# Performance work log

Measured on AMD Instinct MI355X. Metric: run time of the kernel, lower is better.

Reference implementation:

```python
import jax, jax.numpy as jnp
import numpy as np

B, D = 8192, 256      # batch, input_dim == n_nodes
ENC = 256             # encoder_dim
DEC = 64              # decoder_dim
THR = 0.1             # adjacency threshold


def setup_inputs() -> dict:
    key = jax.random.key(0)
    ks = jax.random.split(key, 9)
    s = lambda k, sh, fan: jax.random.normal(k, sh, jnp.float32) / np.sqrt(fan).astype(np.float32)
    return {
        "x": jax.random.normal(ks[0], (B, D), jnp.float32),
        "eps": jax.random.normal(ks[1], (B, D), jnp.float32),
        "W_enc": s(ks[2], (D, ENC), D), "b_enc": jnp.zeros((ENC,), jnp.float32),
        "W_mu": s(ks[3], (ENC, D), ENC), "b_mu": jnp.zeros((D,), jnp.float32),
        "W_lv": s(ks[4], (ENC, D), ENC), "b_lv": jnp.zeros((D,), jnp.float32),
        "graph_param": jax.random.normal(ks[5], (D, D), jnp.float32),
        "W_emb": s(ks[6], (D, DEC), 1), "b_emb": jnp.zeros((D, DEC), jnp.float32),
        "W_g1": s(ks[7], (DEC, DEC // 2), DEC), "b_g1": jnp.zeros((DEC // 2,), jnp.float32),
        "W_g2": s(ks[8], (DEC // 2, 1), DEC // 2), "b_g2": jnp.zeros((1,), jnp.float32),
        "iter_": 100,
    }


def _learned_graph(graph_param, iter_):
    # LearnedGraph.forward: sigmoid, force self-loops=1, threshold after iter 50
    g = jax.nn.sigmoid(graph_param)
    eye = jnp.eye(g.shape[0], dtype=g.dtype)
    g = g * (1.0 - eye) + eye
    if iter_ > 50:  # iter_ is a static Python int
        g = jnp.where(g > THR, g, 0.0)  # nn.Threshold(THR, 0)
    return g


def _gcn_norm(adj):
    # DGL GraphConv(norm='both') with edge_weight: messages weighted by adj values,
    # but degree normalization uses structural (unweighted) edge counts.
    mask = (adj != 0).astype(adj.dtype)
    dout = jnp.maximum(mask.sum(1), 1.0)  # out-degree of src j (row sums)
    din = jnp.maximum(mask.sum(0), 1.0)   # in-degree of dst i (col sums)
    # out[i] = sum_j adj[j,i] * x[j] / sqrt(dout[j] * din[i])  ->  M[dst, src]
    return (adj / jnp.sqrt(dout)[:, None] / jnp.sqrt(din)[None, :]).T


def reference(x, eps, W_enc, b_enc, W_mu, b_mu, W_lv, b_lv,
              graph_param, W_emb, b_emb, W_g1, b_g1, W_g2, b_g2, iter_):
    # VAE encoder (Linear + ReLU, then mu/logvar heads)
    h = jax.nn.relu(x @ W_enc + b_enc)
    mu = h @ W_mu + b_mu
    logvar = h @ W_lv + b_lv
    z = mu + eps * jnp.exp(0.5 * logvar)                 # [B, D]
    # learned adjacency over the D feature-nodes
    adj = _learned_graph(graph_param, iter_)             # [D, D]
    # per-feature node embedding: Linear(1, DEC) + tanh per feature
    b_z = jnp.tanh(z[:, :, None] * W_emb[None] + b_emb[None])  # [B, D, DEC]
    # two GraphConv layers (shared adjacency per batch element)
    M = _gcn_norm(adj)                                   # [D, D]
    h1 = jax.nn.relu(jnp.einsum('ij,bjd->bid', M, b_z) @ W_g1 + b_g1)  # [B, D, 32]
    h2 = jnp.einsum('ij,bjd->bid', M, h1) @ W_g2 + b_g2                # [B, D, 1]
    x_hat = h2.reshape(B, -1)                            # [B, D]
    return x_hat, adj, mu, logvar
```

## Files before the change

kernel.cpp:

```cpp
#include <hip/hip_runtime.h>

typedef __bf16 bf16_t;
typedef __bf16 bf16x4 __attribute__((ext_vector_type(4)));
typedef __bf16 bf16x8 __attribute__((ext_vector_type(8)));
typedef float  floatx4 __attribute__((ext_vector_type(4)));

#define MFMA16(a, b, c) __builtin_amdgcn_mfma_f32_16x16x32_bf16((a), (b), (c), 0, 0, 0)

#define ADJ_OFF  2097152
#define MU_OFF   2162688
#define LV_OFF   4259840

#define TWO_LOG2E 2.8853900817779268f

__device__ __forceinline__ float fast_tanh2(float argE2) {
    float e = __builtin_amdgcn_exp2f(argE2);
    return 1.0f - 2.0f * __builtin_amdgcn_rcpf(e + 1.0f);
}

__device__ __forceinline__ bf16x8 cvt8(const float* p) {
    const floatx4 a = *(const floatx4*)p;
    const floatx4 b = *(const floatx4*)(p + 4);
    bf16x8 r;
#pragma unroll
    for (int j = 0; j < 4; j++) { r[j] = (bf16_t)a[j]; r[4 + j] = (bf16_t)b[j]; }
    return r;
}

__global__ __launch_bounds__(256) void k_prep(
    const float* __restrict__ We, const float* __restrict__ Wm,
    const float* __restrict__ Wl, const float* __restrict__ Wemb,
    const float* __restrict__ bemb, bf16_t* __restrict__ Wt,
    bf16_t* __restrict__ wepack, bf16_t* __restrict__ bepack,
    int* __restrict__ colc) {
    __shared__ float tile[32][33];
    const int b = blockIdx.x, tid = threadIdx.x;
    if (b < 192) {
        const int m = b >> 6, t6 = b & 63;
        const int K0 = (t6 >> 3) << 5, N0 = (t6 & 7) << 5;
        const float* src = (m == 0) ? We : ((m == 1) ? Wm : Wl);
#pragma unroll
        for (int p = 0; p < 4; p++) {
            const int idx = p * 256 + tid;
            tile[idx >> 5][idx & 31] = src[(K0 + (idx >> 5)) * 256 + N0 + (idx & 31)];
        }
        __syncthreads();
        bf16_t* dst = Wt + m * 65536;
#pragma unroll
        for (int p = 0; p < 4; p++) {
            const int idx = p * 256 + tid;
            const int nn = idx >> 5, kk = idx & 31;
            dst[(N0 + nn) * 256 + K0 + kk] = (bf16_t)tile[kk][nn];
        }
    } else if (b < 200) {
        const int base = (b - 192) * 2048;
#pragma unroll
        for (int p = 0; p < 8; p++) {
            const int idx = base + p * 256 + tid;
            wepack[idx] = (bf16_t)(TWO_LOG2E * Wemb[idx]);
        }
    } else {
        if (b == 200) colc[tid] = 0;
        const int base = (b - 200) * 2048;
#pragma unroll
        for (int p = 0; p < 8; p++) {
            const int idx = base + p * 256 + tid;
            bepack[idx] = (bf16_t)(TWO_LOG2E * bemb[idx]);
        }
    }
}

__global__ __launch_bounds__(256) void k_deg(
    const float* __restrict__ gp, const int* __restrict__ iterp,
    int* __restrict__ colc, float* __restrict__ rsO) {
    __shared__ unsigned long long mk[4];
    const int j = blockIdx.x, t = threadIdx.x;
    const bool thr = (*iterp) > 50;
    float g = 1.0f / (1.0f + expf(-gp[j * 256 + t]));
    if (t == j) g = 1.0f;
    if (thr && !(g > 0.1f)) g = 0.0f;
    const bool nz = (g != 0.0f);
    const unsigned long long bal = __ballot(nz);
    if ((t & 63) == 0) mk[t >> 6] = bal;
    if (nz) atomicAdd(&colc[t], 1);
    __syncthreads();
    if (t == 0) {
        const int rc = (int)(__popcll(mk[0]) + __popcll(mk[1]) +
                             __popcll(mk[2]) + __popcll(mk[3]));
        rsO[j] = rsqrtf((float)(rc < 1 ? 1 : rc));
    }
}

__global__ __launch_bounds__(256) void k_mkM(
    const float* __restrict__ gp, const int* __restrict__ iterp,
    const int* __restrict__ colc, const float* __restrict__ rsO,
    bf16_t* __restrict__ Mb, float* __restrict__ adjOut) {
    const int j = blockIdx.x, t = threadIdx.x;
    const int ci = colc[t];
    const float rsi = rsqrtf((float)(ci < 1 ? 1 : ci));
    float g = 1.0f / (1.0f + expf(-gp[j * 256 + t]));
    if (t == j) g = 1.0f;
    if ((*iterp) > 50 && !(g > 0.1f)) g = 0.0f;
    if (adjOut) adjOut[j * 256 + t] = g;
    Mb[t * 256 + j] = (bf16_t)(g * rsO[j] * rsi);
}

__global__ __launch_bounds__(512) void k_ench(
    const float* __restrict__ X, const bf16_t* __restrict__ Wt,
    const float* __restrict__ benc, const float* __restrict__ bmu,
    const float* __restrict__ blv,
    float* __restrict__ MuOut, float* __restrict__ LvOut) {
    __shared__ __align__(16) bf16_t Xs[32 * 264];
    __shared__ __align__(16) bf16_t Hs[32 * 264];
    const bf16_t* Bte = Wt;
    const bf16_t* Btm = Wt + 65536;
    const bf16_t* Btl = Wt + 131072;
    const int tid = threadIdx.x;
    const int r0 = blockIdx.x * 32;
    const int w = tid >> 6;
    const int lane = tid & 63;
    const int n = lane & 15, q = lane >> 4;
    const int cw = w * 32;
    const floatx4 z4 = {0.f, 0.f, 0.f, 0.f};

#pragma unroll
    for (int p = 0; p < 2; p++) {
        const int e0 = (p * 512 + tid) * 8;
        const int row = e0 >> 8, col = e0 & 255;
        *(bf16x8*)(Xs + row * 264 + col) = cvt8(X + (r0 + row) * 256 + col);
    }
    __syncthreads();

    floatx4 ah[2][2];
#pragma unroll
    for (int rt = 0; rt < 2; rt++)
#pragma unroll
        for (int tc = 0; tc < 2; tc++) ah[rt][tc] = z4;
#pragma unroll 2
    for (int k0 = 0; k0 < 256; k0 += 32) {
        bf16x8 a[2], b[2];
#pragma unroll
        for (int rt = 0; rt < 2; rt++)
            a[rt] = *(const bf16x8*)(Xs + (rt * 16 + n) * 264 + k0 + q * 8);
#pragma unroll
        for (int tc = 0; tc < 2; tc++)
            b[tc] = *(const bf16x8*)(Bte + (cw + tc * 16 + n) * 256 + k0 + q * 8);
#pragma unroll
        for (int rt = 0; rt < 2; rt++)
#pragma unroll
            for (int tc = 0; tc < 2; tc++)
                ah[rt][tc] = MFMA16(a[rt], b[tc], ah[rt][tc]);
    }
#pragma unroll
    for (int tc = 0; tc < 2; tc++) {
        const int col = cw + tc * 16 + n;
        const float bv = benc[col];
#pragma unroll
        for (int rt = 0; rt < 2; rt++)
#pragma unroll
            for (int r = 0; r < 4; r++)
                Hs[(rt * 16 + q * 4 + r) * 264 + col] =
                    (bf16_t)fmaxf(ah[rt][tc][r] + bv, 0.0f);
    }
    __syncthreads();

    floatx4 am[2][2], al[2][2];
#pragma unroll
    for (int rt = 0; rt < 2; rt++)
#pragma unroll
        for (int tc = 0; tc < 2; tc++) { am[rt][tc] = z4; al[rt][tc] = z4; }
#pragma unroll 2
    for (int k0 = 0; k0 < 256; k0 += 32) {
        bf16x8 a[2], bm_[2], bl_[2];
#pragma unroll
        for (int rt = 0; rt < 2; rt++)
            a[rt] = *(const bf16x8*)(Hs + (rt * 16 + n) * 264 + k0 + q * 8);
#pragma unroll
        for (int tc = 0; tc < 2; tc++) {
            bm_[tc] = *(const bf16x8*)(Btm + (cw + tc * 16 + n) * 256 + k0 + q * 8);
            bl_[tc] = *(const bf16x8*)(Btl + (cw + tc * 16 + n) * 256 + k0 + q * 8);
        }
#pragma unroll
        for (int rt = 0; rt < 2; rt++)
#pragma unroll
            for (int tc = 0; tc < 2; tc++) {
                am[rt][tc] = MFMA16(a[rt], bm_[tc], am[rt][tc]);
                al[rt][tc] = MFMA16(a[rt], bl_[tc], al[rt][tc]);
            }
    }
#pragma unroll
    for (int tc = 0; tc < 2; tc++) {
        const int col = cw + tc * 16 + n;
        const float bmv = bmu[col], blvv = blv[col];
#pragma unroll
        for (int rt = 0; rt < 2; rt++)
#pragma unroll
            for (int r = 0; r < 4; r++) {
                const int row = r0 + rt * 16 + q * 4 + r;
                MuOut[row * 256 + col] = am[rt][tc][r] + bmv;
                LvOut[row * 256 + col] = al[rt][tc][r] + blvv;
            }
    }
}

__global__ __launch_bounds__(512, 4) void k_gcn(
    const float* __restrict__ Mu, const float* __restrict__ Lv,
    const float* __restrict__ Eps, const bf16_t* __restrict__ wepack,
    const bf16_t* __restrict__ bepack, const float* __restrict__ Wg1,
    const float* __restrict__ bg1, const float* __restrict__ Wg2,
    const bf16_t* __restrict__ Mb, float* __restrict__ Vout) {
    __shared__ __align__(16) bf16_t smem[128 * 256];
    __shared__ float zs[1024];
    const int tid = threadIdx.x;
    const int lane = tid & 63;
    const int w = tid >> 6;
    const int n = lane & 15, q = lane >> 4;
    const int bg = blockIdx.x;
    const floatx4 z4 = {0.f, 0.f, 0.f, 0.f};

    {
        const int gi = bg * 1024 + tid;
        zs[tid] = fmaf(Eps[gi], __expf(0.5f * Lv[gi]), Mu[gi]);
        const int gi2 = gi + 512;
        zs[tid + 512] = fmaf(Eps[gi2], __expf(0.5f * Lv[gi2]), Mu[gi2]);
    }

    bf16x8 wg1f[2][2];
#pragma unroll
    for (int ks = 0; ks < 2; ks++)
#pragma unroll
        for (int te = 0; te < 2; te++)
#pragma unroll
            for (int j = 0; j < 8; j++)
                wg1f[ks][te][j] = (bf16_t)Wg1[(ks * 32 + q * 8 + j) * 32 + te * 16 + n];
    __syncthreads();

#pragma unroll
    for (int jt2 = 0; jt2 < 2; jt2++) {
        const int j0 = (w * 2 + jt2) * 16;
        const int jA = j0 + n;
        const bf16x8 we0 = *(const bf16x8*)(wepack + jA * 64 + q * 8);
        const bf16x8 we1 = *(const bf16x8*)(wepack + jA * 64 + 32 + q * 8);
        const bf16x8 be0 = *(const bf16x8*)(bepack + jA * 64 + q * 8);
        const bf16x8 be1 = *(const bf16x8*)(bepack + jA * 64 + 32 + q * 8);
        float wf0[8], wf1[8], bf0[8], bf1[8];
#pragma unroll
        for (int j = 0; j < 8; j++) {
            wf0[j] = (float)we0[j]; wf1[j] = (float)we1[j];
            bf0[j] = (float)be0[j]; bf1[j] = (float)be1[j];
        }
        const int j8a = (j0 >> 3) + (q >> 1);
        const int jlo = (q & 1) * 4;
        const int sw = ((j8a ^ (n & 7)) << 3) + jlo;
#pragma unroll
        for (int bl = 0; bl < 4; bl++) {
            const float zv = zs[bl * 256 + jA];
            bf16x8 a0, a1;
#pragma unroll
            for (int j = 0; j < 8; j++) {
                a0[j] = (bf16_t)fast_tanh2(fmaf(zv, wf0[j], bf0[j]));
                a1[j] = (bf16_t)fast_tanh2(fmaf(zv, wf1[j], bf1[j]));
            }
            floatx4 c0 = z4, c1 = z4;
            c0 = MFMA16(a0, wg1f[0][0], c0);
            c0 = MFMA16(a1, wg1f[1][0], c0);
            c1 = MFMA16(a0, wg1f[0][1], c1);
            c1 = MFMA16(a1, wg1f[1][1], c1);
            bf16x4 s0, s1;
#pragma unroll
            for (int r = 0; r < 4; r++) { s0[r] = (bf16_t)c0[r]; s1[r] = (bf16_t)c1[r]; }
            *(bf16x4*)(smem + (bl * 32 + n) * 256 + sw) = s0;
            *(bf16x4*)(smem + (bl * 32 + 16 + n) * 256 + sw) = s1;
        }
    }
    __syncthreads();

    const int i0 = w * 32;
    floatx4 acc[2][8];
#pragma unroll
    for (int ti = 0; ti < 2; ti++)
#pragma unroll
        for (int tc = 0; tc < 8; tc++) acc[ti][tc] = z4;
#pragma unroll
    for (int k0 = 0; k0 < 256; k0 += 32) {
        const int k8 = k0 >> 3;
        bf16x8 a[2], b[8];
#pragma unroll
        for (int ti = 0; ti < 2; ti++)
            a[ti] = *(const bf16x8*)(Mb + (i0 + ti * 16 + n) * 256 + k0 + q * 8);
#pragma unroll
        for (int tc = 0; tc < 8; tc++)
            b[tc] = *(const bf16x8*)(smem + (tc * 16 + n) * 256 +
                                     (((k8 + q) ^ (n & 7)) << 3));
        __builtin_amdgcn_s_setprio(1);
#pragma unroll
        for (int ti = 0; ti < 2; ti++)
#pragma unroll
            for (int tc = 0; tc < 8; tc++)
                acc[ti][tc] = MFMA16(a[ti], b[tc], acc[ti][tc]);
        __builtin_amdgcn_s_setprio(0);
    }

    const float w2a = Wg2[n],      w2b = Wg2[16 + n];
    const float b1a = bg1[n],      b1b = bg1[16 + n];
    float v32[32];
#pragma unroll
    for (int bl = 0; bl < 4; bl++)
#pragma unroll
        for (int ti = 0; ti < 2; ti++)
#pragma unroll
            for (int r = 0; r < 4; r++)
                v32[bl * 8 + ti * 4 + r] =
                    fmaxf(acc[ti][2 * bl][r] + b1a, 0.0f) * w2a +
                    fmaxf(acc[ti][2 * bl + 1][r] + b1b, 0.0f) * w2b;
    const bool h0 = (lane & 1), h1_ = (lane & 2), h2 = (lane & 4), h3 = (lane & 8);
    float u16[16];
#pragma unroll
    for (int p = 0; p < 16; p++) {
        const float keep = h0 ? v32[2 * p + 1] : v32[2 * p];
        const float send = h0 ? v32[2 * p] : v32[2 * p + 1];
        u16[p] = keep + __shfl_xor(send, 1, 64);
    }
    float u8[8];
#pragma unroll
    for (int p = 0; p < 8; p++) {
        const float keep = h1_ ? u16[2 * p + 1] : u16[2 * p];
        const float send = h1_ ? u16[2 * p] : u16[2 * p + 1];
        u8[p] = keep + __shfl_xor(send, 2, 64);
    }
    float u4[4];
#pragma unroll
    for (int p = 0; p < 4; p++) {
        const float keep = h2 ? u8[2 * p + 1] : u8[2 * p];
        const float send = h2 ? u8[2 * p] : u8[2 * p + 1];
        u4[p] = keep + __shfl_xor(send, 4, 64);
    }
    float u2[2];
#pragma unroll
    for (int p = 0; p < 2; p++) {
        const float keep = h3 ? u4[2 * p + 1] : u4[2 * p];
        const float send = h3 ? u4[2 * p] : u4[2 * p + 1];
        u2[p] = keep + __shfl_xor(send, 8, 64);
    }
    {
        const int i_out = i0 + ((n >> 2) & 1) * 16 + q * 4 + (n & 3);
        const int blv = n >> 3;
        Vout[bg * 1024 + blv * 256 + i_out] = u2[0];
        Vout[bg * 1024 + (2 + blv) * 256 + i_out] = u2[1];
    }
}

__global__ __launch_bounds__(512) void k_out(
    float* __restrict__ VX, const bf16_t* __restrict__ Mb,
    const float* __restrict__ bg2) {
    __shared__ __align__(16) bf16_t va[32 * 264];
    const int tid = threadIdx.x;
    const int lane = tid & 63;
    const int w = tid >> 6;
    const int n = lane & 15, q = lane >> 4;
    const int r0 = blockIdx.x * 32;

#pragma unroll
    for (int p = 0; p < 4; p++) {
        const int i4 = p * 512 + tid;
        const int row = i4 >> 6, c4 = (i4 & 63) * 4;
        const floatx4 v = *(const floatx4*)(VX + (r0 + row) * 256 + c4);
        bf16x4 s;
#pragma unroll
        for (int r = 0; r < 4; r++) s[r] = (bf16_t)v[r];
        *(bf16x4*)(va + row * 264 + c4) = s;
    }
    __syncthreads();

    const int cw = w * 32;
    const floatx4 z4 = {0.f, 0.f, 0.f, 0.f};
    floatx4 acc[2][2];
#pragma unroll
    for (int rt = 0; rt < 2; rt++)
#pragma unroll
        for (int tc = 0; tc < 2; tc++) acc[rt][tc] = z4;
#pragma unroll 2
    for (int k0 = 0; k0 < 256; k0 += 32) {
        bf16x8 a[2], b[2];
#pragma unroll
        for (int rt = 0; rt < 2; rt++)
            a[rt] = *(const bf16x8*)(va + (rt * 16 + n) * 264 + k0 + q * 8);
#pragma unroll
        for (int tc = 0; tc < 2; tc++)
            b[tc] = *(const bf16x8*)(Mb + (cw + tc * 16 + n) * 256 + k0 + q * 8);
#pragma unroll
        for (int rt = 0; rt < 2; rt++)
#pragma unroll
            for (int tc = 0; tc < 2; tc++)
                acc[rt][tc] = MFMA16(a[rt], b[tc], acc[rt][tc]);
    }
    const float bv = bg2[0];
#pragma unroll
    for (int tc = 0; tc < 2; tc++) {
        const int col = cw + tc * 16 + n;
#pragma unroll
        for (int rt = 0; rt < 2; rt++)
#pragma unroll
            for (int r = 0; r < 4; r++)
                VX[(r0 + rt * 16 + q * 4 + r) * 256 + col] = acc[rt][tc][r] + bv;
    }
}

__global__ __launch_bounds__(256) void k_adj(
    const float* __restrict__ gp, const int* __restrict__ iterp,
    float* __restrict__ adjOut) {
    const int o = blockIdx.x * 256 + threadIdx.x;
    const int j = o >> 8, i = o & 255;
    float g = 1.0f / (1.0f + expf(-gp[o]));
    if (i == j) g = 1.0f;
    if ((*iterp) > 50 && !(g > 0.1f)) g = 0.0f;
    adjOut[o] = g;
}

extern "C" void kernel_launch(void* const* d_in, const int* in_sizes, int n_in,
                              void* d_out, int out_size, void* d_ws, size_t ws_size,
                              hipStream_t stream) {
    const float* x    = (const float*)d_in[0];
    const float* eps  = (const float*)d_in[1];
    const float* Wenc = (const float*)d_in[2];
    const float* benc = (const float*)d_in[3];
    const float* Wmu  = (const float*)d_in[4];
    const float* bmu  = (const float*)d_in[5];
    const float* Wlv  = (const float*)d_in[6];
    const float* blv  = (const float*)d_in[7];
    const float* gp   = (const float*)d_in[8];
    const float* Wemb = (const float*)d_in[9];
    const float* bemb = (const float*)d_in[10];
    const float* Wg1  = (const float*)d_in[11];
    const float* bg1  = (const float*)d_in[12];
    const float* Wg2  = (const float*)d_in[13];
    const float* bg2  = (const float*)d_in[14];
    const int*   itr  = (const int*)d_in[15];
    (void)in_sizes; (void)n_in; (void)out_size;

    float* xhat = (float*)d_out;
    float* adjO = xhat + ADJ_OFF;
    float* muo  = xhat + MU_OFF;
    float* lvo  = xhat + LV_OFF;

    const bool usews = (d_ws != nullptr && ws_size >= 262144);
    char* scr = usews ? (char*)d_ws : (char*)adjO;
    bf16_t* Mb     = (bf16_t*)scr;
    bf16_t* wepack = (bf16_t*)(scr + 131072);
    bf16_t* bepack = (bf16_t*)(scr + 163840);
    int*    colc   = (int*)(scr + 196608);
    float*  rsO    = (float*)(scr + 197632);
    bf16_t* Wt     = (bf16_t*)((char*)d_out + 4194304);

    k_prep<<<dim3(208), dim3(256), 0, stream>>>(Wenc, Wmu, Wlv, Wemb, bemb,
                                                Wt, wepack, bepack, colc);
    k_deg <<<dim3(256), dim3(256), 0, stream>>>(gp, itr, colc, rsO);
    k_mkM <<<dim3(256), dim3(256), 0, stream>>>(gp, itr, colc, rsO, Mb,
                                                usews ? adjO : nullptr);
    k_ench<<<dim3(256), dim3(512), 0, stream>>>(x, Wt, benc, bmu, blv, muo, lvo);
    k_gcn <<<dim3(2048), dim3(512), 0, stream>>>(muo, lvo, eps, wepack, bepack,
                                                 Wg1, bg1, Wg2, Mb, xhat);
    k_out <<<dim3(256), dim3(512), 0, stream>>>(xhat, Mb, bg2);
    if (!usews)
        k_adj<<<dim3(256), dim3(256), 0, stream>>>(gp, itr, adjO);
}
```

Before: 192.5 us.

## Fuse second graph aggregation into GCN kernel and fold degree pass into prep

The final M·h2 aggregation is folded into k_gcn: each block now keeps its four per-row values in shared memory and runs the 256×256 multiply with MFMA there, instead of writing Vout to global memory and re-reading it in a separate k_out kernel. The degree computation kernel is merged into k_prep as extra blocks that write per-row ballot bitmasks. k_mkM then derives row and column counts from those bitmasks, which removes the global atomics. Trade-offs: each k_gcn block re-reads part of Mb for only 4 rows, so MFMA utilisation is low there, and k_mkM repeats a 256-step column count in every block.

```diff
diff --git a/kernel.cpp b/kernel.cpp
--- a/kernel.cpp
+++ b/kernel.cpp
@@ -4,6 +4,7 @@
 typedef __bf16 bf16x4 __attribute__((ext_vector_type(4)));
 typedef __bf16 bf16x8 __attribute__((ext_vector_type(8)));
 typedef float  floatx4 __attribute__((ext_vector_type(4)));
+typedef unsigned long long u64;
 
 #define MFMA16(a, b, c) __builtin_amdgcn_mfma_f32_16x16x32_bf16((a), (b), (c), 0, 0, 0)
 
@@ -30,9 +31,10 @@
 __global__ __launch_bounds__(256) void k_prep(
     const float* __restrict__ We, const float* __restrict__ Wm,
     const float* __restrict__ Wl, const float* __restrict__ Wemb,
-    const float* __restrict__ bemb, bf16_t* __restrict__ Wt,
+    const float* __restrict__ bemb, const float* __restrict__ gp,
+    const int* __restrict__ iterp, bf16_t* __restrict__ Wt,
     bf16_t* __restrict__ wepack, bf16_t* __restrict__ bepack,
-    int* __restrict__ colc) {
+    u64* __restrict__ rowbits) {
     __shared__ float tile[32][33];
     const int b = blockIdx.x, tid = threadIdx.x;
     if (b < 192) {
@@ -59,50 +61,50 @@
             const int idx = base + p * 256 + tid;
             wepack[idx] = (bf16_t)(TWO_LOG2E * Wemb[idx]);
         }
-    } else {
-        if (b == 200) colc[tid] = 0;
+    } else if (b < 208) {
         const int base = (b - 200) * 2048;
 #pragma unroll
         for (int p = 0; p < 8; p++) {
             const int idx = base + p * 256 + tid;
             bepack[idx] = (bf16_t)(TWO_LOG2E * bemb[idx]);
         }
-    }
-}
-
-__global__ __launch_bounds__(256) void k_deg(
-    const float* __restrict__ gp, const int* __restrict__ iterp,
-    int* __restrict__ colc, float* __restrict__ rsO) {
-    __shared__ unsigned long long mk[4];
-    const int j = blockIdx.x, t = threadIdx.x;
-    const bool thr = (*iterp) > 50;
-    float g = 1.0f / (1.0f + expf(-gp[j * 256 + t]));
-    if (t == j) g = 1.0f;
-    if (thr && !(g > 0.1f)) g = 0.0f;
-    const bool nz = (g != 0.0f);
-    const unsigned long long bal = __ballot(nz);
-    if ((t & 63) == 0) mk[t >> 6] = bal;
-    if (nz) atomicAdd(&colc[t], 1);
-    __syncthreads();
-    if (t == 0) {
-        const int rc = (int)(__popcll(mk[0]) + __popcll(mk[1]) +
-                             __popcll(mk[2]) + __popcll(mk[3]));
-        rsO[j] = rsqrtf((float)(rc < 1 ? 1 : rc));
+    } else {
+        const int j = b - 208;
+        const bool thr = (*iterp) > 50;
+        float g = 1.0f / (1.0f + expf(-gp[j * 256 + tid]));
+        if (tid == j) g = 1.0f;
+        if (thr && !(g > 0.1f)) g = 0.0f;
+        const u64 bal = __ballot(g != 0.0f);
+        if ((tid & 63) == 0) rowbits[j * 4 + (tid >> 6)] = bal;
     }
 }
 
 __global__ __launch_bounds__(256) void k_mkM(
     const float* __restrict__ gp, const int* __restrict__ iterp,
-    const int* __restrict__ colc, const float* __restrict__ rsO,
-    bf16_t* __restrict__ Mb, float* __restrict__ adjOut) {
+    const u64* __restrict__ rowbits, bf16_t* __restrict__ Mb,
+    float* __restrict__ adjOut) {
+    __shared__ u64 bits[256][4];
     const int j = blockIdx.x, t = threadIdx.x;
-    const int ci = colc[t];
-    const float rsi = rsqrtf((float)(ci < 1 ? 1 : ci));
+#pragma unroll
+    for (int p = 0; p < 4; p++) {
+        const int idx = p * 256 + t;
+        bits[idx >> 2][idx & 3] = rowbits[idx];
+    }
+    __syncthreads();
+    const int w64 = t >> 6, sh = t & 63;
+    int cnt = 0;
+#pragma unroll 8
+    for (int jp = 0; jp < 256; jp++)
+        cnt += (int)((bits[jp][w64] >> sh) & 1ull);
+    const int rc = (int)(__popcll(bits[j][0]) + __popcll(bits[j][1]) +
+                         __popcll(bits[j][2]) + __popcll(bits[j][3]));
+    const float rso = rsqrtf((float)(rc < 1 ? 1 : rc));
+    const float rsi = rsqrtf((float)(cnt < 1 ? 1 : cnt));
     float g = 1.0f / (1.0f + expf(-gp[j * 256 + t]));
     if (t == j) g = 1.0f;
     if ((*iterp) > 50 && !(g > 0.1f)) g = 0.0f;
     if (adjOut) adjOut[j * 256 + t] = g;
-    Mb[t * 256 + j] = (bf16_t)(g * rsO[j] * rsi);
+    Mb[t * 256 + j] = (bf16_t)(g * rso * rsi);
 }
 
 __global__ __launch_bounds__(512) void k_ench(
@@ -208,8 +210,10 @@
     const float* __restrict__ Eps, const bf16_t* __restrict__ wepack,
     const bf16_t* __restrict__ bepack, const float* __restrict__ Wg1,
     const float* __restrict__ bg1, const float* __restrict__ Wg2,
-    const bf16_t* __restrict__ Mb, float* __restrict__ Vout) {
+    const bf16_t* __restrict__ Mb, const float* __restrict__ bg2,
+    float* __restrict__ xhat) {
     __shared__ __align__(16) bf16_t smem[128 * 256];
+    __shared__ __align__(16) bf16_t Vs[4 * 256];
     __shared__ float zs[1024];
     const int tid = threadIdx.x;
     const int lane = tid & 63;
@@ -243,12 +247,6 @@
         const bf16x8 we1 = *(const bf16x8*)(wepack + jA * 64 + 32 + q * 8);
         const bf16x8 be0 = *(const bf16x8*)(bepack + jA * 64 + q * 8);
         const bf16x8 be1 = *(const bf16x8*)(bepack + jA * 64 + 32 + q * 8);
-        float wf0[8], wf1[8], bf0[8], bf1[8];
-#pragma unroll
-        for (int j = 0; j < 8; j++) {
-            wf0[j] = (float)we0[j]; wf1[j] = (float)we1[j];
-            bf0[j] = (float)be0[j]; bf1[j] = (float)be1[j];
-        }
         const int j8a = (j0 >> 3) + (q >> 1);
         const int jlo = (q & 1) * 4;
         const int sw = ((j8a ^ (n & 7)) << 3) + jlo;
@@ -258,8 +256,8 @@
             bf16x8 a0, a1;
 #pragma unroll
             for (int j = 0; j < 8; j++) {
-                a0[j] = (bf16_t)fast_tanh2(fmaf(zv, wf0[j], bf0[j]));
-                a1[j] = (bf16_t)fast_tanh2(fmaf(zv, wf1[j], bf1[j]));
+                a0[j] = (bf16_t)fast_tanh2(fmaf(zv, (float)we0[j], (float)be0[j]));
+                a1[j] = (bf16_t)fast_tanh2(fmaf(zv, (float)we1[j], (float)be1[j]));
             }
             floatx4 c0 = z4, c1 = z4;
             c0 = MFMA16(a0, wg1f[0][0], c0);
@@ -345,64 +343,33 @@
     {
         const int i_out = i0 + ((n >> 2) & 1) * 16 + q * 4 + (n & 3);
         const int blv = n >> 3;
-        Vout[bg * 1024 + blv * 256 + i_out] = u2[0];
-        Vout[bg * 1024 + (2 + blv) * 256 + i_out] = u2[1];
-    }
-}
-
-__global__ __launch_bounds__(512) void k_out(
-    float* __restrict__ VX, const bf16_t* __restrict__ Mb,
-    const float* __restrict__ bg2) {
-    __shared__ __align__(16) bf16_t va[32 * 264];
-    const int tid = threadIdx.x;
-    const int lane = tid & 63;
-    const int w = tid >> 6;
-    const int n = lane & 15, q = lane >> 4;
-    const int r0 = blockIdx.x * 32;
-
-#pragma unroll
-    for (int p = 0; p < 4; p++) {
-        const int i4 = p * 512 + tid;
-        const int row = i4 >> 6, c4 = (i4 & 63) * 4;
-        const floatx4 v = *(const floatx4*)(VX + (r0 + row) * 256 + c4);
-        bf16x4 s;
-#pragma unroll
-        for (int r = 0; r < 4; r++) s[r] = (bf16_t)v[r];
-        *(bf16x4*)(va + row * 264 + c4) = s;
-    }
-    __syncthreads();
-
-    const int cw = w * 32;
-    const floatx4 z4 = {0.f, 0.f, 0.f, 0.f};
-    floatx4 acc[2][2];
-#pragma unroll
-    for (int rt = 0; rt < 2; rt++)
-#pragma unroll
-        for (int tc = 0; tc < 2; tc++) acc[rt][tc] = z4;
-#pragma unroll 2
-    for (int k0 = 0; k0 < 256; k0 += 32) {
-        bf16x8 a[2], b[2];
-#pragma unroll
-        for (int rt = 0; rt < 2; rt++)
-            a[rt] = *(const bf16x8*)(va + (rt * 16 + n) * 264 + k0 + q * 8);
-#pragma unroll
-        for (int tc = 0; tc < 2; tc++)
-            b[tc] = *(const bf16x8*)(Mb + (cw + tc * 16 + n) * 256 + k0 + q * 8);
-#pragma unroll
-        for (int rt = 0; rt < 2; rt++)
+        Vs[blv * 256 + i_out] = (bf16_t)u2[0];
+        Vs[(2 + blv) * 256 + i_out] = (bf16_t)u2[1];
+    }
+    __syncthreads();
+
+    {
+        floatx4 acc3[2];
+        acc3[0] = z4; acc3[1] = z4;
+#pragma unroll
+        for (int k0 = 0; k0 < 256; k0 += 32) {
+            const bf16x8 a3 = *(const bf16x8*)(Vs + (n & 3) * 256 + k0 + q * 8);
+            bf16x8 b3[2];
 #pragma unroll
             for (int tc = 0; tc < 2; tc++)
-                acc[rt][tc] = MFMA16(a[rt], b[tc], acc[rt][tc]);
-    }
-    const float bv = bg2[0];
-#pragma unroll
-    for (int tc = 0; tc < 2; tc++) {
-        const int col = cw + tc * 16 + n;
-#pragma unroll
-        for (int rt = 0; rt < 2; rt++)
-#pragma unroll
-            for (int r = 0; r < 4; r++)
-                VX[(r0 + rt * 16 + q * 4 + r) * 256 + col] = acc[rt][tc][r] + bv;
+                b3[tc] = *(const bf16x8*)(Mb + (i0 + tc * 16 + n) * 256 + k0 + q * 8);
+#pragma unroll
+            for (int tc = 0; tc < 2; tc++)
+                acc3[tc] = MFMA16(a3, b3[tc], acc3[tc]);
+        }
+        const float bv = bg2[0];
+        if (q == 0) {
+#pragma unroll
+            for (int tc = 0; tc < 2; tc++)
+#pragma unroll
+                for (int r = 0; r < 4; r++)
+                    xhat[(bg * 4 + r) * 256 + i0 + tc * 16 + n] = acc3[tc][r] + bv;
+        }
     }
 }
 
@@ -445,22 +412,20 @@
 
     const bool usews = (d_ws != nullptr && ws_size >= 262144);
     char* scr = usews ? (char*)d_ws : (char*)adjO;
-    bf16_t* Mb     = (bf16_t*)scr;
-    bf16_t* wepack = (bf16_t*)(scr + 131072);
-    bf16_t* bepack = (bf16_t*)(scr + 163840);
-    int*    colc   = (int*)(scr + 196608);
-    float*  rsO    = (float*)(scr + 197632);
-    bf16_t* Wt     = (bf16_t*)((char*)d_out + 4194304);
-
-    k_prep<<<dim3(208), dim3(256), 0, stream>>>(Wenc, Wmu, Wlv, Wemb, bemb,
-                                                Wt, wepack, bepack, colc);
-    k_deg <<<dim3(256), dim3(256), 0, stream>>>(gp, itr, colc, rsO);
-    k_mkM <<<dim3(256), dim3(256), 0, stream>>>(gp, itr, colc, rsO, Mb,
+    bf16_t* Mb      = (bf16_t*)scr;
+    bf16_t* wepack  = (bf16_t*)(scr + 131072);
+    bf16_t* bepack  = (bf16_t*)(scr + 163840);
+    u64*    rowbits = (u64*)(scr + 196608);
+    bf16_t* Wt      = (bf16_t*)((char*)d_out + 4194304);
+
+    k_prep<<<dim3(464), dim3(256), 0, stream>>>(Wenc, Wmu, Wlv, Wemb, bemb,
+                                                gp, itr, Wt, wepack, bepack,
+                                                rowbits);
+    k_mkM <<<dim3(256), dim3(256), 0, stream>>>(gp, itr, rowbits, Mb,
                                                 usews ? adjO : nullptr);
     k_ench<<<dim3(256), dim3(512), 0, stream>>>(x, Wt, benc, bmu, blv, muo, lvo);
     k_gcn <<<dim3(2048), dim3(512), 0, stream>>>(muo, lvo, eps, wepack, bepack,
-                                                 Wg1, bg1, Wg2, Mb, xhat);
-    k_out <<<dim3(256), dim3(512), 0, stream>>>(xhat, Mb, bg2);
+                                                 Wg1, bg1, Wg2, Mb, bg2, xhat);
     if (!usews)
         k_adj<<<dim3(256), dim3(256), 0, stream>>>(gp, itr, adjO);
 }
```

Measured after the change: 207.0 us. 1.08x slower.
